# Performance work log

Hardware: AMD Instinct MI355X
Metric: run time of the kernel (lower is better)

The kernel has to match this reference:

```python
import jax, jax.numpy as jnp
import numpy as np
import math

QUERY_DIM = 128
SCALE = 1.0 / math.sqrt(QUERY_DIM)

def setup_inputs() -> dict:
    key = jax.random.key(0)
    k1, k2, k3 = jax.random.split(key, 3)
    B, Q, K, D = 16, 2048, 2048, 128
    return {
        "query": jax.random.normal(k1, (B, Q, D), dtype=jnp.float32),
        "keys": jax.random.normal(k2, (B, K, D), dtype=jnp.float32),
        "values": jax.random.normal(k3, (B, K, D), dtype=jnp.float32),
    }

def reference(query, keys, values):
    # energy[b,q,k] = sum_d query[b,q,d] * keys[b,k,d], scaled then softmax over k
    energy = jnp.einsum("bqd,bkd->bqk", query, keys) * SCALE
    attn = jax.nn.softmax(energy, axis=2)
    # linear combination over values
    return jnp.einsum("bqk,bkv->bqv", attn, values)
```

## Files before the change

### kernel.cpp

```cpp
#include <hip/hip_runtime.h>
#include <hip/hip_bf16.h>


#define BATCH 16
#define QLEN 2048
#define KLEN 2048
#define DIM 128
#define BM 64
#define BN 64
#define NT (KLEN / BN)

#define KBYTES 16384
#define BUFBYTES 32768

typedef __attribute__((ext_vector_type(8))) short bf16x8;
typedef __attribute__((ext_vector_type(4))) float f32x4;

__device__ __forceinline__ short f2bf(float x) {
    union { float f; unsigned u; } v; v.f = x;
    unsigned r = v.u + 0x7FFFu + ((v.u >> 16) & 1u);
    return (short)(r >> 16);
}
__device__ __forceinline__ unsigned pkbf(float a, float b) {
    union { float f; unsigned u; } x, y; x.f = a; y.f = b;
    unsigned ra = x.u + 0x7FFFu + ((x.u >> 16) & 1u);
    unsigned rb = y.u + 0x7FFFu + ((y.u >> 16) & 1u);
    return __builtin_amdgcn_perm(rb, ra, 0x07060302u);
}

#define GLOAD_LDS16(g, l) \
    __builtin_amdgcn_global_load_lds((__attribute__((address_space(1))) void*)(g), \
                                     (__attribute__((address_space(3))) void*)(l), 16, 0, 0)

#define TSTR 72
__global__ __launch_bounds__(256) void prepass_kernel(
    const float* __restrict__ kg, const float* __restrict__ vg,
    unsigned short* __restrict__ Kws, unsigned short* __restrict__ Vtws)
{
    __shared__ unsigned short T[DIM * TSTR];
    const int tid = threadIdx.x;
    const int kb  = blockIdx.x * BN;
    const int b   = blockIdx.y;
    const float* kt = kg + ((size_t)b * KLEN + kb) * DIM;
    const float* vt = vg + ((size_t)b * KLEN + kb) * DIM;
    unsigned short* ko = Kws + ((size_t)b * KLEN + kb) * DIM;
#pragma unroll
    for (int j = 0; j < 8; ++j) {
        int idx = tid + 256 * j;
        int key = idx >> 5;
        int d4  = (idx & 31) * 4;
        float4 kv = *(const float4*)(kt + key * DIM + d4);
        uint2 w; w.x = pkbf(kv.x, kv.y); w.y = pkbf(kv.z, kv.w);
        *(uint2*)(ko + key * DIM + d4) = w;
        float4 vv = *(const float4*)(vt + key * DIM + d4);
        T[(d4 + 0) * TSTR + key] = (unsigned short)f2bf(vv.x);
        T[(d4 + 1) * TSTR + key] = (unsigned short)f2bf(vv.y);
        T[(d4 + 2) * TSTR + key] = (unsigned short)f2bf(vv.z);
        T[(d4 + 3) * TSTR + key] = (unsigned short)f2bf(vv.w);
    }
    __syncthreads();
    unsigned short* vo = Vtws + (size_t)b * DIM * KLEN + kb;
#pragma unroll
    for (int j = 0; j < 4; ++j) {
        int c = tid + 256 * j;
        int d = c >> 3;
        int g = c & 7;
        uint4 u = *(const uint4*)&T[d * TSTR + g * 8];
        *(uint4*)(vo + (size_t)d * KLEN + g * 8) = u;
    }
}

__global__ __launch_bounds__(512, 4) void attn_flash_kernel(
    const float* __restrict__ qg,
    const unsigned short* __restrict__ Kws,
    const unsigned short* __restrict__ Vtws,
    float* __restrict__ outg)
{
    __shared__ __align__(16) char SMC[2 * BUFBYTES];

    const int tid  = threadIdx.x;
    const int wave = tid >> 6;
    const int lane = tid & 63;
    const int lm   = lane & 15;
    const int quad = lane >> 4;
    const int rw   = wave >> 1;
    const int kw   = wave & 1;

    const int n  = blockIdx.y * gridDim.x + blockIdx.x;
    const int np = (n & 7) * 64 + (n >> 3);
    const int b     = np >> 5;
    const int qbase = (np & 31) * BM + rw * 16;

    const float QSCALE = 0.08838834764831845f * 1.4426950408889634f;

    bf16x8 qf[4];
    {
        const float* qrow = qg + (size_t)(b * QLEN + qbase + lm) * DIM;
#pragma unroll
        for (int dk = 0; dk < 4; ++dk) {
            int d0 = dk * 32 + quad * 8;
            float4 a = *(const float4*)(qrow + d0);
            float4 c = *(const float4*)(qrow + d0 + 4);
            uint4 u;
            u.x = pkbf(a.x*QSCALE, a.y*QSCALE); u.y = pkbf(a.z*QSCALE, a.w*QSCALE);
            u.z = pkbf(c.x*QSCALE, c.y*QSCALE); u.w = pkbf(c.z*QSCALE, c.w*QSCALE);
            qf[dk] = *(bf16x8*)&u;
        }
    }

    f32x4 O[8];
#pragma unroll
    for (int i = 0; i < 8; ++i) O[i] = 0.0f;
    float lr = 0.f;

    const unsigned short* Kb  = Kws  + (size_t)b * KLEN * DIM;
    const unsigned short* Vtb = Vtws + (size_t)b * DIM * KLEN;
    const char* kdma[2];
    const char* vdma[2];
    {
        int gk  = lane & 15;
        int r0  = wave * 8 + (lane >> 4);
        int gv  = lane & 7;
        int d0v = wave * 16 + (lane >> 3);
#pragma unroll
        for (int i = 0; i < 2; ++i) {
            int r = r0 + 4 * i;
            int key = (r & 3) | ((r & 4) << 1) | ((r & 8) << 1) | ((r & 16) >> 2) | (r & 32);
            kdma[i] = (const char*)Kb + key * 256 + ((gk ^ (r & 15)) << 4);
            int dv = d0v + 8 * i;
            vdma[i] = (const char*)Vtb + (size_t)dv * (KLEN * 2) + ((gv ^ (dv & 7)) << 4);
        }
    }

    int kfo[4];
#pragma unroll
    for (int dk = 0; dk < 4; ++dk)
        kfo[dk] = (kw * 32 + lm) * 256 + (((dk * 4 + quad) ^ lm) << 4);
    const int vfo = lm * 128 + (((kw * 4 + quad) ^ (lm & 7)) << 4);

    auto dma = [&](int tt, int bb) {
        char* ldsK = SMC + bb * BUFBYTES + wave * 2048;
        char* ldsV = SMC + bb * BUFBYTES + KBYTES + wave * 2048;
        size_t ko = (size_t)tt * 16384;
        size_t vo = (size_t)tt * 128;
#pragma unroll
        for (int i = 0; i < 2; ++i) {
            GLOAD_LDS16(kdma[i] + ko, ldsK + i * 1024);
            GLOAD_LDS16(vdma[i] + vo, ldsV + i * 1024);
        }
    };

    dma(0, 0);
    __syncthreads();

    for (int t = 0; t < NT; ++t) {
        if (t + 1 < NT) dma(t + 1, (t + 1) & 1);

        const char* bufK = SMC + (t & 1) * BUFBYTES;
        const char* bufV = bufK + KBYTES;

        f32x4 S0 = 0.0f, S1 = 0.0f;
#pragma unroll
        for (int dk = 0; dk < 4; ++dk) {
            bf16x8 kf0 = *(const bf16x8*)(bufK + kfo[dk]);
            bf16x8 kf1 = *(const bf16x8*)(bufK + kfo[dk] + 4096);
            S0 = __builtin_amdgcn_mfma_f32_16x16x32_bf16(kf0, qf[dk], S0, 0, 0, 0);
            S1 = __builtin_amdgcn_mfma_f32_16x16x32_bf16(kf1, qf[dk], S1, 0, 0, 0);
        }

        float a0 = exp2f(S0[0]), a1 = exp2f(S0[1]), a2 = exp2f(S0[2]), a3 = exp2f(S0[3]);
        float a4 = exp2f(S1[0]), a5 = exp2f(S1[1]), a6 = exp2f(S1[2]), a7 = exp2f(S1[3]);
        uint4 pu;
        pu.x = pkbf(a0,a1); pu.y = pkbf(a2,a3); pu.z = pkbf(a4,a5); pu.w = pkbf(a6,a7);
        bf16x8 pf = *(bf16x8*)&pu;
        lr += ((a0+a1)+(a2+a3)) + ((a4+a5)+(a6+a7));

#pragma unroll
        for (int dt = 0; dt < 8; ++dt) {
            bf16x8 vf = *(const bf16x8*)(bufV + vfo + dt * 2048);
            O[dt] = __builtin_amdgcn_mfma_f32_16x16x32_bf16(vf, pf, O[dt], 0, 0, 0);
        }

        __syncthreads();
    }

    lr += __shfl_xor(lr, 16, 64);
    lr += __shfl_xor(lr, 32, 64);

    float* Orw = (float*)SMC + rw * 2128;
    if (kw == 1) {
#pragma unroll
        for (int dt = 0; dt < 8; ++dt)
            *(f32x4*)&Orw[lm * 132 + dt * 16 + quad * 4] = O[dt];
        if (lane < 16) Orw[2112 + lm] = lr;
    }
    __syncthreads();
    if (kw == 0) {
        float inv = 1.0f / (lr + Orw[2112 + lm]);
        float* orow = outg + (size_t)(b * QLEN + qbase + lm) * DIM;
#pragma unroll
        for (int dt = 0; dt < 8; ++dt) {
            f32x4 o = *(const f32x4*)&Orw[lm * 132 + dt * 16 + quad * 4];
            *(f32x4*)&orow[dt * 16 + quad * 4] = (O[dt] + o) * inv;
        }
    }
}

extern "C" void kernel_launch(void* const* d_in, const int* in_sizes, int n_in,
                              void* d_out, int out_size, void* d_ws, size_t ws_size,
                              hipStream_t stream) {
    const float* q = (const float*)d_in[0];
    const float* k = (const float*)d_in[1];
    const float* v = (const float*)d_in[2];
    float* o = (float*)d_out;
    unsigned short* Kws  = (unsigned short*)d_ws;
    unsigned short* Vtws = Kws + (size_t)BATCH * KLEN * DIM;
    dim3 grid(KLEN / BN, BATCH);
    prepass_kernel<<<grid, 256, 0, stream>>>(k, v, Kws, Vtws);
    dim3 grid2(QLEN / BM, BATCH);
    attn_flash_kernel<<<grid2, 512, 0, stream>>>(q, Kws, Vtws, o);
}
```

Baseline: 141.7 us.

## Rework wave split so each wave covers 32 queries and 16 keys

Waves are reorganized from 4 query-row groups x 2 key splits to 2 query-row groups x 4 key splits. Each wave now holds two 16-row query tiles and reuses one K fragment across both QK MFMAs, then uses 16x16x16 MFMAs for PV so one V fragment feeds both tiles. The intent is to cut LDS fragment reads per MFMA. In exchange it doubles accumulator registers and needs a three-step serial LDS reduction at the end. The V prepass now swizzles its transposed read and the K DMA drops its key permutation.

```diff
diff --git a/kernel.cpp b/kernel.cpp
--- a/kernel.cpp
+++ b/kernel.cpp
@@ -14,6 +14,7 @@
 #define BUFBYTES 32768
 
 typedef __attribute__((ext_vector_type(8))) short bf16x8;
+typedef __attribute__((ext_vector_type(4))) short bf16x4;
 typedef __attribute__((ext_vector_type(4))) float f32x4;
 
 __device__ __forceinline__ short f2bf(float x) {
@@ -65,7 +66,8 @@
         int c = tid + 256 * j;
         int d = c >> 3;
         int g = c & 7;
-        uint4 u = *(const uint4*)&T[d * TSTR + g * 8];
+        int cl = g ^ (d & 7);
+        uint4 u = *(const uint4*)&T[d * TSTR + cl * 8];
         *(uint4*)(vo + (size_t)d * KLEN + g * 8) = u;
     }
 }
@@ -83,40 +85,46 @@
     const int lane = tid & 63;
     const int lm   = lane & 15;
     const int quad = lane >> 4;
-    const int rw   = wave >> 1;
-    const int kw   = wave & 1;
+    const int rw   = wave >> 2;
+    const int kw   = wave & 3;
 
     const int n  = blockIdx.y * gridDim.x + blockIdx.x;
     const int np = (n & 7) * 64 + (n >> 3);
     const int b     = np >> 5;
-    const int qbase = (np & 31) * BM + rw * 16;
+    const int qbase = (np & 31) * BM + rw * 32;
 
     const float QSCALE = 0.08838834764831845f * 1.4426950408889634f;
 
-    bf16x8 qf[4];
+    bf16x8 qfA[4], qfB[4];
     {
-        const float* qrow = qg + (size_t)(b * QLEN + qbase + lm) * DIM;
+        const float* qrowA = qg + (size_t)(b * QLEN + qbase + lm) * DIM;
+        const float* qrowB = qrowA + 16 * DIM;
 #pragma unroll
         for (int dk = 0; dk < 4; ++dk) {
             int d0 = dk * 32 + quad * 8;
-            float4 a = *(const float4*)(qrow + d0);
-            float4 c = *(const float4*)(qrow + d0 + 4);
+            float4 a = *(const float4*)(qrowA + d0);
+            float4 c = *(const float4*)(qrowA + d0 + 4);
             uint4 u;
             u.x = pkbf(a.x*QSCALE, a.y*QSCALE); u.y = pkbf(a.z*QSCALE, a.w*QSCALE);
             u.z = pkbf(c.x*QSCALE, c.y*QSCALE); u.w = pkbf(c.z*QSCALE, c.w*QSCALE);
-            qf[dk] = *(bf16x8*)&u;
-        }
-    }
-
-    f32x4 O[8];
-#pragma unroll
-    for (int i = 0; i < 8; ++i) O[i] = 0.0f;
-    float lr = 0.f;
-
-    const unsigned short* Kb  = Kws  + (size_t)b * KLEN * DIM;
-    const unsigned short* Vtb = Vtws + (size_t)b * DIM * KLEN;
-    const char* kdma[2];
-    const char* vdma[2];
+            qfA[dk] = *(bf16x8*)&u;
+            float4 e = *(const float4*)(qrowB + d0);
+            float4 g = *(const float4*)(qrowB + d0 + 4);
+            uint4 v;
+            v.x = pkbf(e.x*QSCALE, e.y*QSCALE); v.y = pkbf(e.z*QSCALE, e.w*QSCALE);
+            v.z = pkbf(g.x*QSCALE, g.y*QSCALE); v.w = pkbf(g.z*QSCALE, g.w*QSCALE);
+            qfB[dk] = *(bf16x8*)&v;
+        }
+    }
+
+    f32x4 OA[8], OB[8];
+#pragma unroll
+    for (int i = 0; i < 8; ++i) { OA[i] = 0.0f; OB[i] = 0.0f; }
+    float lrA = 0.f, lrB = 0.f;
+
+    const char* Kb  = (const char*)(Kws  + (size_t)b * KLEN * DIM);
+    const char* Vtb = (const char*)(Vtws + (size_t)b * DIM * KLEN);
+    int kOff[2], vOff[2];
     {
         int gk  = lane & 15;
         int r0  = wave * 8 + (lane >> 4);
@@ -125,28 +133,28 @@
 #pragma unroll
         for (int i = 0; i < 2; ++i) {
             int r = r0 + 4 * i;
-            int key = (r & 3) | ((r & 4) << 1) | ((r & 8) << 1) | ((r & 16) >> 2) | (r & 32);
-            kdma[i] = (const char*)Kb + key * 256 + ((gk ^ (r & 15)) << 4);
+            kOff[i] = r * 256 + ((gk ^ (r & 15)) << 4);
             int dv = d0v + 8 * i;
-            vdma[i] = (const char*)Vtb + (size_t)dv * (KLEN * 2) + ((gv ^ (dv & 7)) << 4);
+            vOff[i] = dv * (KLEN * 2) + (gv << 4);
         }
     }
 
     int kfo[4];
 #pragma unroll
     for (int dk = 0; dk < 4; ++dk)
-        kfo[dk] = (kw * 32 + lm) * 256 + (((dk * 4 + quad) ^ lm) << 4);
-    const int vfo = lm * 128 + (((kw * 4 + quad) ^ (lm & 7)) << 4);
+        kfo[dk] = (kw * 16 + lm) * 256 + (((dk * 4 + quad) ^ lm) << 4);
+    const int vfo0 = lm * 128 + ((((kw * 2) + (quad >> 1)) ^ (lm & 7)) << 4)
+                   + ((quad & 1) << 3);
 
     auto dma = [&](int tt, int bb) {
         char* ldsK = SMC + bb * BUFBYTES + wave * 2048;
         char* ldsV = SMC + bb * BUFBYTES + KBYTES + wave * 2048;
-        size_t ko = (size_t)tt * 16384;
-        size_t vo = (size_t)tt * 128;
+        int ko = tt * 16384;
+        int vo = tt * 128;
 #pragma unroll
         for (int i = 0; i < 2; ++i) {
-            GLOAD_LDS16(kdma[i] + ko, ldsK + i * 1024);
-            GLOAD_LDS16(vdma[i] + vo, ldsV + i * 1024);
+            GLOAD_LDS16(Kb + kOff[i] + ko, ldsK + i * 1024);
+            GLOAD_LDS16(Vtb + vOff[i] + vo, ldsV + i * 1024);
         }
     };
 
@@ -159,49 +167,72 @@
         const char* bufK = SMC + (t & 1) * BUFBYTES;
         const char* bufV = bufK + KBYTES;
 
-        f32x4 S0 = 0.0f, S1 = 0.0f;
+        f32x4 SA = 0.0f, SB = 0.0f;
 #pragma unroll
         for (int dk = 0; dk < 4; ++dk) {
-            bf16x8 kf0 = *(const bf16x8*)(bufK + kfo[dk]);
-            bf16x8 kf1 = *(const bf16x8*)(bufK + kfo[dk] + 4096);
-            S0 = __builtin_amdgcn_mfma_f32_16x16x32_bf16(kf0, qf[dk], S0, 0, 0, 0);
-            S1 = __builtin_amdgcn_mfma_f32_16x16x32_bf16(kf1, qf[dk], S1, 0, 0, 0);
-        }
-
-        float a0 = exp2f(S0[0]), a1 = exp2f(S0[1]), a2 = exp2f(S0[2]), a3 = exp2f(S0[3]);
-        float a4 = exp2f(S1[0]), a5 = exp2f(S1[1]), a6 = exp2f(S1[2]), a7 = exp2f(S1[3]);
-        uint4 pu;
-        pu.x = pkbf(a0,a1); pu.y = pkbf(a2,a3); pu.z = pkbf(a4,a5); pu.w = pkbf(a6,a7);
-        bf16x8 pf = *(bf16x8*)&pu;
-        lr += ((a0+a1)+(a2+a3)) + ((a4+a5)+(a6+a7));
+            bf16x8 kf = *(const bf16x8*)(bufK + kfo[dk]);
+            SA = __builtin_amdgcn_mfma_f32_16x16x32_bf16(kf, qfA[dk], SA, 0, 0, 0);
+            SB = __builtin_amdgcn_mfma_f32_16x16x32_bf16(kf, qfB[dk], SB, 0, 0, 0);
+        }
+
+        float a0 = exp2f(SA[0]), a1 = exp2f(SA[1]), a2 = exp2f(SA[2]), a3 = exp2f(SA[3]);
+        float b0 = exp2f(SB[0]), b1 = exp2f(SB[1]), b2 = exp2f(SB[2]), b3 = exp2f(SB[3]);
+        uint2 puA, puB;
+        puA.x = pkbf(a0, a1); puA.y = pkbf(a2, a3);
+        puB.x = pkbf(b0, b1); puB.y = pkbf(b2, b3);
+        bf16x4 pfA = *(bf16x4*)&puA;
+        bf16x4 pfB = *(bf16x4*)&puB;
+        lrA += (a0 + a1) + (a2 + a3);
+        lrB += (b0 + b1) + (b2 + b3);
 
 #pragma unroll
         for (int dt = 0; dt < 8; ++dt) {
-            bf16x8 vf = *(const bf16x8*)(bufV + vfo + dt * 2048);
-            O[dt] = __builtin_amdgcn_mfma_f32_16x16x32_bf16(vf, pf, O[dt], 0, 0, 0);
+            bf16x4 vf = *(const bf16x4*)(bufV + vfo0 + dt * 2048);
+            OA[dt] = __builtin_amdgcn_mfma_f32_16x16x16bf16_1k(vf, pfA, OA[dt], 0, 0, 0);
+            OB[dt] = __builtin_amdgcn_mfma_f32_16x16x16bf16_1k(vf, pfB, OB[dt], 0, 0, 0);
         }
 
         __syncthreads();
     }
 
-    lr += __shfl_xor(lr, 16, 64);
-    lr += __shfl_xor(lr, 32, 64);
-
-    float* Orw = (float*)SMC + rw * 2128;
-    if (kw == 1) {
-#pragma unroll
-        for (int dt = 0; dt < 8; ++dt)
-            *(f32x4*)&Orw[lm * 132 + dt * 16 + quad * 4] = O[dt];
-        if (lane < 16) Orw[2112 + lm] = lr;
-    }
-    __syncthreads();
+    lrA += __shfl_xor(lrA, 16, 64); lrA += __shfl_xor(lrA, 32, 64);
+    lrB += __shfl_xor(lrB, 16, 64); lrB += __shfl_xor(lrB, 32, 64);
+
+#define OSTR 132
+#define RSZ  (32 * OSTR + 32)
+    float* R = (float*)SMC + rw * RSZ;
+#pragma unroll
+    for (int s = 3; s >= 1; --s) {
+        if (kw == s) {
+#pragma unroll
+            for (int dt = 0; dt < 8; ++dt) {
+                *(f32x4*)&R[lm * OSTR        + dt * 16 + quad * 4] = OA[dt];
+                *(f32x4*)&R[(16 + lm) * OSTR + dt * 16 + quad * 4] = OB[dt];
+            }
+            if (lane < 16)      R[32 * OSTR + lm]      = lrA;
+            else if (lane < 32) R[32 * OSTR + 16 + lm] = lrB;
+        }
+        __syncthreads();
+        if (kw == s - 1) {
+#pragma unroll
+            for (int dt = 0; dt < 8; ++dt) {
+                OA[dt] += *(const f32x4*)&R[lm * OSTR        + dt * 16 + quad * 4];
+                OB[dt] += *(const f32x4*)&R[(16 + lm) * OSTR + dt * 16 + quad * 4];
+            }
+            lrA += R[32 * OSTR + lm];
+            lrB += R[32 * OSTR + 16 + lm];
+        }
+    }
+
     if (kw == 0) {
-        float inv = 1.0f / (lr + Orw[2112 + lm]);
-        float* orow = outg + (size_t)(b * QLEN + qbase + lm) * DIM;
+        float invA = 1.0f / lrA;
+        float invB = 1.0f / lrB;
+        float* orowA = outg + (size_t)(b * QLEN + qbase + lm) * DIM;
+        float* orowB = orowA + 16 * DIM;
 #pragma unroll
         for (int dt = 0; dt < 8; ++dt) {
-            f32x4 o = *(const f32x4*)&Orw[lm * 132 + dt * 16 + quad * 4];
-            *(f32x4*)&orow[dt * 16 + quad * 4] = (O[dt] + o) * inv;
+            *(f32x4*)&orowA[dt * 16 + quad * 4] = OA[dt] * invA;
+            *(f32x4*)&orowB[dt * 16 + quad * 4] = OB[dt] * invB;
         }
     }
 }
```

Result: slower. 153.2 us (+8.2%).

## Load V fragments directly from global memory instead of staging through LDS

Applied to the files above, without the earlier changes.

Removes the V tile from the LDS double buffer and has each wave read its V MFMA fragments straight from global memory into registers. The reads are split around the QK^T MFMAs to hide latency. This cuts LDS use roughly in half, which may allow more resident blocks, and drops the V LDS reads. In exchange, V is re-read from global/L2 by every row-wave with strided 16-byte accesses, and load latency sits inside the main loop without cross-iteration prefetch.

```diff
diff --git a/kernel.cpp b/kernel.cpp
--- a/kernel.cpp
+++ b/kernel.cpp
@@ -11,7 +11,7 @@
 #define NT (KLEN / BN)
 
 #define KBYTES 16384
-#define BUFBYTES 32768
+#define SMEM_BYTES 34048
 
 typedef __attribute__((ext_vector_type(8))) short bf16x8;
 typedef __attribute__((ext_vector_type(4))) float f32x4;
@@ -76,7 +76,7 @@
     const unsigned short* __restrict__ Vtws,
     float* __restrict__ outg)
 {
-    __shared__ __align__(16) char SMC[2 * BUFBYTES];
+    __shared__ __align__(16) char SMC[SMEM_BYTES];
 
     const int tid  = threadIdx.x;
     const int wave = tid >> 6;
@@ -113,41 +113,33 @@
     for (int i = 0; i < 8; ++i) O[i] = 0.0f;
     float lr = 0.f;
 
-    const unsigned short* Kb  = Kws  + (size_t)b * KLEN * DIM;
-    const unsigned short* Vtb = Vtws + (size_t)b * DIM * KLEN;
+    const unsigned short* Kb = Kws + (size_t)b * KLEN * DIM;
     const char* kdma[2];
-    const char* vdma[2];
     {
-        int gk  = lane & 15;
-        int r0  = wave * 8 + (lane >> 4);
-        int gv  = lane & 7;
-        int d0v = wave * 16 + (lane >> 3);
+        int gk = lane & 15;
+        int r0 = wave * 8 + (lane >> 4);
 #pragma unroll
         for (int i = 0; i < 2; ++i) {
             int r = r0 + 4 * i;
             int key = (r & 3) | ((r & 4) << 1) | ((r & 8) << 1) | ((r & 16) >> 2) | (r & 32);
             kdma[i] = (const char*)Kb + key * 256 + ((gk ^ (r & 15)) << 4);
-            int dv = d0v + 8 * i;
-            vdma[i] = (const char*)Vtb + (size_t)dv * (KLEN * 2) + ((gv ^ (dv & 7)) << 4);
-        }
-    }
+        }
+    }
+
+    const char* vB = (const char*)(Vtws + (size_t)b * DIM * KLEN)
+                   + (size_t)lm * (KLEN * 2) + kw * 64 + quad * 16;
 
     int kfo[4];
 #pragma unroll
     for (int dk = 0; dk < 4; ++dk)
         kfo[dk] = (kw * 32 + lm) * 256 + (((dk * 4 + quad) ^ lm) << 4);
-    const int vfo = lm * 128 + (((kw * 4 + quad) ^ (lm & 7)) << 4);
 
     auto dma = [&](int tt, int bb) {
-        char* ldsK = SMC + bb * BUFBYTES + wave * 2048;
-        char* ldsV = SMC + bb * BUFBYTES + KBYTES + wave * 2048;
-        size_t ko = (size_t)tt * 16384;
-        size_t vo = (size_t)tt * 128;
-#pragma unroll
-        for (int i = 0; i < 2; ++i) {
+        char* ldsK = SMC + bb * KBYTES + wave * 2048;
+        int ko = tt * 16384;
+#pragma unroll
+        for (int i = 0; i < 2; ++i)
             GLOAD_LDS16(kdma[i] + ko, ldsK + i * 1024);
-            GLOAD_LDS16(vdma[i] + vo, ldsV + i * 1024);
-        }
     };
 
     dma(0, 0);
@@ -156,8 +148,13 @@
     for (int t = 0; t < NT; ++t) {
         if (t + 1 < NT) dma(t + 1, (t + 1) & 1);
 
-        const char* bufK = SMC + (t & 1) * BUFBYTES;
-        const char* bufV = bufK + KBYTES;
+        const char* vt = vB + (size_t)t * 128;
+        bf16x8 vf[8];
+#pragma unroll
+        for (int dt = 0; dt < 4; ++dt)
+            vf[dt] = *(const bf16x8*)(vt + (size_t)dt * 65536);
+
+        const char* bufK = SMC + (t & 1) * KBYTES;
 
         f32x4 S0 = 0.0f, S1 = 0.0f;
 #pragma unroll
@@ -167,6 +164,10 @@
             S0 = __builtin_amdgcn_mfma_f32_16x16x32_bf16(kf0, qf[dk], S0, 0, 0, 0);
             S1 = __builtin_amdgcn_mfma_f32_16x16x32_bf16(kf1, qf[dk], S1, 0, 0, 0);
         }
+
+#pragma unroll
+        for (int dt = 4; dt < 8; ++dt)
+            vf[dt] = *(const bf16x8*)(vt + (size_t)dt * 65536);
 
         float a0 = exp2f(S0[0]), a1 = exp2f(S0[1]), a2 = exp2f(S0[2]), a3 = exp2f(S0[3]);
         float a4 = exp2f(S1[0]), a5 = exp2f(S1[1]), a6 = exp2f(S1[2]), a7 = exp2f(S1[3]);
@@ -176,10 +177,8 @@
         lr += ((a0+a1)+(a2+a3)) + ((a4+a5)+(a6+a7));
 
 #pragma unroll
-        for (int dt = 0; dt < 8; ++dt) {
-            bf16x8 vf = *(const bf16x8*)(bufV + vfo + dt * 2048);
-            O[dt] = __builtin_amdgcn_mfma_f32_16x16x32_bf16(vf, pf, O[dt], 0, 0, 0);
-        }
+        for (int dt = 0; dt < 8; ++dt)
+            O[dt] = __builtin_amdgcn_mfma_f32_16x16x32_bf16(vf[dt], pf, O[dt], 0, 0, 0);
 
         __syncthreads();
     }
```

New measurement: 217.4 us. 1.53x slower.
